# Performance work log

Hardware: AMD Instinct MI355X
Metric: run time of the kernel (lower is better)

## Reference

```python
import jax, jax.numpy as jnp
import numpy as np

N_NODES = 50000
N_EDGES = 800000
N_GRAPHS = 256
C_FEAT = 108
MLP_DIM = 88
OUT_DIM = 100


def setup_inputs() -> dict:
    key = jax.random.key(0)
    ks = jax.random.split(key, 12)
    x = jax.random.normal(ks[0], (N_NODES, C_FEAT), dtype=jnp.float32)
    edge_index = jax.random.randint(ks[1], (2, N_EDGES), 0, N_NODES, dtype=jnp.int64)
    batch = jnp.sort(jax.random.randint(ks[2], (N_NODES,), 0, N_GRAPHS, dtype=jnp.int64))

    def glorot(k, shape):
        fan_in, fan_out = shape
        s = jnp.sqrt(2.0 / (fan_in + fan_out))
        return jax.random.normal(k, shape, dtype=jnp.float32) * s

    return {
        "x": x,
        "edge_index": edge_index,
        "batch": batch,
        # SAGEConv layer 1: lin_l (neighbors, has bias), lin_r (root, no bias)
        "W1l": glorot(ks[3], (C_FEAT, MLP_DIM)),
        "W1r": glorot(ks[4], (C_FEAT, MLP_DIM)),
        "b1": jnp.zeros((MLP_DIM,), jnp.float32),
        "W2l": glorot(ks[5], (MLP_DIM, MLP_DIM)),
        "W2r": glorot(ks[6], (MLP_DIM, MLP_DIM)),
        "b2": jnp.zeros((MLP_DIM,), jnp.float32),
        "W3l": glorot(ks[7], (MLP_DIM, MLP_DIM)),
        "W3r": glorot(ks[8], (MLP_DIM, MLP_DIM)),
        "b3": jnp.zeros((MLP_DIM,), jnp.float32),
        "Wlin": glorot(ks[9], (MLP_DIM, OUT_DIM)),
        "blin": jnp.zeros((OUT_DIM,), jnp.float32),
    }


def _sage_conv(x, src, dst, Wl, Wr, b):
    """PyG SAGEConv(aggr='mean'): out = lin_l(mean_j x_j) + lin_r(x)."""
    n = x.shape[0]
    msg = x[src]  # [E, d] gather from source nodes
    agg = jax.ops.segment_sum(msg, dst, num_segments=n)  # [N, d]
    cnt = jax.ops.segment_sum(jnp.ones((src.shape[0],), x.dtype), dst, num_segments=n)
    agg = agg / jnp.maximum(cnt, 1.0)[:, None]  # scatter-mean
    return agg @ Wl + b + x @ Wr


def reference(x, edge_index, batch, W1l, W1r, b1, W2l, W2r, b2, W3l, W3r, b3, Wlin, blin):
    src, dst = edge_index[0], edge_index[1]
    h = jax.nn.relu(_sage_conv(x, src, dst, W1l, W1r, b1))
    h = jax.nn.relu(_sage_conv(h, src, dst, W2l, W2r, b2))
    h = jax.nn.relu(_sage_conv(h, src, dst, W3l, W3r, b3))
    pooled = jax.ops.segment_sum(h, batch, num_segments=N_GRAPHS)  # global_add_pool
    return pooled @ Wlin + blin  # [n_graphs, 100]
```

## Files before the change

### kernel.cpp

```cpp
#include <hip/hip_runtime.h>
#include <hip/hip_fp16.h>

#define NN 50000
#define NG 256
#define CF 108
#define MD 88
#define OD 100
#define F2 44
#define HP 96
#define HP2 48
#define YLS 96
#define K1P 128
#define NSB 196
#define SBCAP 5120
#define TILE 2048
#define NCH 12

typedef _Float16 f16x8 __attribute__((ext_vector_type(8)));
typedef float f32x4 __attribute__((ext_vector_type(4)));


__global__ __launch_bounds__(256) void prep_kernel(const int* __restrict__ edge, int E,
                                                   int* __restrict__ sbcur,
                                                   unsigned* __restrict__ sbrec,
                                                   const float* __restrict__ x,
                                                   _Float16* __restrict__ xh, int N,
                                                   const float* __restrict__ W1l, const float* __restrict__ W1r,
                                                   const float* __restrict__ W2l, const float* __restrict__ W2r,
                                                   const float* __restrict__ W3l, const float* __restrict__ W3r,
                                                   _Float16* __restrict__ Wct1, _Float16* __restrict__ Wct23,
                                                   int nbin, int nconvx) {
    const int tid = threadIdx.x;
    const int bb  = blockIdx.x;

    if (bb < nbin) {
        __shared__ int bcnt[NSB], boff[NSB], bfill[NSB], gbase[NSB];
        __shared__ int sc[256];
        __shared__ unsigned stag[TILE];
        __shared__ unsigned char stagbin[TILE];
        const int t0  = bb * TILE;
        const int tcnt = min(TILE, E - t0);

        for (int i = tid; i < NSB; i += 256) bcnt[i] = 0;
        __syncthreads();

        unsigned recs[TILE / 256];
        int      bins[TILE / 256];
        #pragma unroll
        for (int j = 0; j < TILE / 256; ++j) {
            const int e = t0 + j * 256 + tid;
            bins[j] = -1;
            if (e < E) {
                const int dst = edge[E + e], src = edge[e];
                bins[j] = dst >> 8;
                recs[j] = ((unsigned)src << 8) | (unsigned)(dst & 255);
                atomicAdd(&bcnt[bins[j]], 1);
            }
        }
        __syncthreads();

        sc[tid] = (tid < NSB) ? bcnt[tid] : 0;
        __syncthreads();
        for (int d = 1; d < 256; d <<= 1) {
            int v = (tid >= d) ? sc[tid - d] : 0;
            __syncthreads();
            sc[tid] += v;
            __syncthreads();
        }
        if (tid < NSB) {
            boff[tid]  = sc[tid] - bcnt[tid];
            bfill[tid] = sc[tid] - bcnt[tid];
            if (bcnt[tid] > 0) gbase[tid] = atomicAdd(&sbcur[tid], bcnt[tid]);
        }
        __syncthreads();

        #pragma unroll
        for (int j = 0; j < TILE / 256; ++j) {
            if (bins[j] >= 0) {
                int pos = atomicAdd(&bfill[bins[j]], 1);
                stag[pos]    = recs[j];
                stagbin[pos] = (unsigned char)bins[j];
            }
        }
        __syncthreads();

        for (int i = tid; i < tcnt; i += 256) {
            const int b   = stagbin[i];
            const int rel = i - boff[b];
            const int gp  = gbase[b] + rel;
            if (gp < SBCAP) sbrec[(size_t)b * SBCAP + gp] = stag[i];
        }
    } else if (bb < nbin + nconvx) {
        const int i = (bb - nbin) * 256 + tid;
        if (i < N * K1P) {
            int n = i >> 7, k = i & (K1P - 1);
            xh[i] = (k < CF) ? (_Float16)x[n * CF + k] : (_Float16)0.f;
        }
    } else {
        const int n1 = 176 * K1P;
        const int n2 = 176 * HP;
        const int idx = (bb - nbin - nconvx) * 256 + tid;
        if (idx < n1) {
            int c = idx / K1P, k = idx - c * K1P;
            float v = (k < CF) ? ((c < MD) ? W1l[k * MD + c] : W1r[k * MD + (c - MD)]) : 0.f;
            Wct1[idx] = (_Float16)v;
        } else if (idx < n1 + 2 * n2) {
            int j = idx - n1;
            const float* Wl = (j < n2) ? W2l : W3l;
            const float* Wr = (j < n2) ? W2r : W3r;
            int jj = (j < n2) ? j : j - n2;
            int c = jj / HP, k = jj - c * HP;
            float v = (k < MD) ? ((c < MD) ? Wl[k * MD + c] : Wr[k * MD + (c - MD)]) : 0.f;
            Wct23[j] = (_Float16)v;
        }
    }
}


__global__ __launch_bounds__(256) void csr256_kernel(const unsigned* __restrict__ sbrec,
                                                     const int* __restrict__ sbcur,
                                                     int* __restrict__ csr,
                                                     int2* __restrict__ off2,
                                                     int* __restrict__ order, int N) {
    __shared__ int hist[256], base[256], offc[256], sc[256];
    __shared__ int dcnt[64], dpos[64];
    const int b = blockIdx.x, tid = threadIdx.x;
    const int cnt = min(sbcur[b], SBCAP);
    const unsigned* rec = sbrec + (size_t)b * SBCAP;

    hist[tid] = 0;
    if (tid < 64) dcnt[tid] = 0;
    __syncthreads();
    for (int r = tid; r < cnt; r += 256) atomicAdd(&hist[rec[r] & 255u], 1);
    __syncthreads();

    sc[tid] = hist[tid];
    __syncthreads();
    for (int d = 1; d < 256; d <<= 1) {
        int v = (tid >= d) ? sc[tid - d] : 0;
        __syncthreads();
        sc[tid] += v;
        __syncthreads();
    }
    base[tid] = sc[tid] - hist[tid];
    offc[tid] = base[tid];
    __syncthreads();

    for (int r = tid; r < cnt; r += 256) {
        const unsigned u = rec[r];
        const int dl = (int)(u & 255u);
        const int pos = atomicAdd(&offc[dl], 1);
        csr[(size_t)b * SBCAP + pos] = (int)(u >> 8);
    }

    const int n = b * 256 + tid;
    const int deg = (n < N) ? min(hist[tid], 63) : 63;
    atomicAdd(&dcnt[deg], 1);
    __syncthreads();
    if (tid < 64) {
        int v = dcnt[tid];
        int incl = v;
        #pragma unroll
        for (int s = 1; s < 64; s <<= 1) {
            int t = __shfl_up(incl, s, 64);
            if (tid >= s) incl += t;
        }
        dpos[tid] = incl - v;
    }
    __syncthreads();
    const int rank = atomicAdd(&dpos[deg], 1);
    order[b * 256 + rank] = (n < N) ? n : -1;

    if (n < N) off2[n] = make_int2(b * SBCAP + base[tid], hist[tid]);
}


template <int KPAD>
__global__ __launch_bounds__(256) void gemm_mfma_kernel(const _Float16* __restrict__ Ah,
                                                        const _Float16* __restrict__ Wct,
                                                        const float* __restrict__ bias,
                                                        _Float16* __restrict__ yl,
                                                        _Float16* __restrict__ yr, int N) {
    const int wave = threadIdx.x >> 6;
    const int lane = threadIdx.x & 63;
    const int r16  = lane & 15;
    const int kg   = lane >> 4;
    const int rbase = blockIdx.x * 128 + wave * 16;

    const int arow0 = min(rbase + r16, N - 1);
    const int arow1 = min(rbase + 64 + r16, N - 1);
    const _Float16* ap0 = Ah + (size_t)arow0 * KPAD + kg * 8;
    const _Float16* ap1 = Ah + (size_t)arow1 * KPAD + kg * 8;

    f32x4 acc[2][11];
    #pragma unroll
    for (int q = 0; q < 2; ++q)
        #pragma unroll
        for (int t = 0; t < 11; ++t) acc[q][t] = (f32x4){0.f, 0.f, 0.f, 0.f};

    #pragma unroll
    for (int ks = 0; ks < KPAD / 32; ++ks) {
        f16x8 af0 = *(const f16x8*)(ap0 + ks * 32);
        f16x8 af1 = *(const f16x8*)(ap1 + ks * 32);
        #pragma unroll
        for (int t = 0; t < 11; ++t) {
            const _Float16* bp = Wct + (size_t)(t * 16 + r16) * KPAD + ks * 32 + kg * 8;
            f16x8 bf = *(const f16x8*)bp;
            acc[0][t] = __builtin_amdgcn_mfma_f32_16x16x32_f16(af0, bf, acc[0][t], 0, 0, 0);
            acc[1][t] = __builtin_amdgcn_mfma_f32_16x16x32_f16(af1, bf, acc[1][t], 0, 0, 0);
        }
    }

    #pragma unroll
    for (int q = 0; q < 2; ++q) {
        const int orow0 = rbase + q * 64 + kg * 4;
        #pragma unroll
        for (int t = 0; t < 11; ++t) {
            const int c = t * 16 + r16;
            const bool isr = (c >= MD);
            const float bv = isr ? bias[c - MD] : 0.f;
            _Float16* dst = isr ? (yr + (c - MD)) : (yl + c);
            const int st = isr ? MD : YLS;
            #pragma unroll
            for (int r = 0; r < 4; ++r) {
                const int row = orow0 + r;
                if (row < N) dst[(size_t)row * st] = (_Float16)(acc[q][t][r] + bv);
            }
        }
    }
}


__global__ void agg_kernel(const _Float16* __restrict__ yl, const _Float16* __restrict__ yr,
                           const int2* __restrict__ off2, const int* __restrict__ csr,
                           const int* __restrict__ order,
                           _Float16* __restrict__ h, int total) {
    int idx = blockIdx.x * blockDim.x + threadIdx.x;
    if (idx >= total) return;
    int slot = idx / NCH;
    int c = idx - slot * NCH;
    const int n = order[slot];
    if (n < 0) return;
    if (c >= 11) {
        *(f16x8*)(h + (size_t)n * HP + 88) = (f16x8)(_Float16)0.f;
        return;
    }
    const int2 o = off2[n];
    const int s = o.x, e = o.x + o.y;
    float a0[8] = {0,0,0,0,0,0,0,0}, a1[8] = {0,0,0,0,0,0,0,0};
    float a2[8] = {0,0,0,0,0,0,0,0}, a3[8] = {0,0,0,0,0,0,0,0};
    const size_t cof = (size_t)c * 8;
    int i = s;
    for (; i + 7 < e; i += 8) {
        f16x8 v0 = *(const f16x8*)(yl + (size_t)csr[i]     * YLS + cof);
        f16x8 v1 = *(const f16x8*)(yl + (size_t)csr[i + 1] * YLS + cof);
        f16x8 v2 = *(const f16x8*)(yl + (size_t)csr[i + 2] * YLS + cof);
        f16x8 v3 = *(const f16x8*)(yl + (size_t)csr[i + 3] * YLS + cof);
        f16x8 v4 = *(const f16x8*)(yl + (size_t)csr[i + 4] * YLS + cof);
        f16x8 v5 = *(const f16x8*)(yl + (size_t)csr[i + 5] * YLS + cof);
        f16x8 v6 = *(const f16x8*)(yl + (size_t)csr[i + 6] * YLS + cof);
        f16x8 v7 = *(const f16x8*)(yl + (size_t)csr[i + 7] * YLS + cof);
        #pragma unroll
        for (int j = 0; j < 8; ++j) {
            a0[j] += (float)v0[j] + (float)v1[j];
            a1[j] += (float)v2[j] + (float)v3[j];
            a2[j] += (float)v4[j] + (float)v5[j];
            a3[j] += (float)v6[j] + (float)v7[j];
        }
    }
    for (; i + 1 < e; i += 2) {
        f16x8 v0 = *(const f16x8*)(yl + (size_t)csr[i]     * YLS + cof);
        f16x8 v1 = *(const f16x8*)(yl + (size_t)csr[i + 1] * YLS + cof);
        #pragma unroll
        for (int j = 0; j < 8; ++j) {
            a0[j] += (float)v0[j];
            a1[j] += (float)v1[j];
        }
    }
    if (i < e) {
        f16x8 v0 = *(const f16x8*)(yl + (size_t)csr[i] * YLS + cof);
        #pragma unroll
        for (int j = 0; j < 8; ++j) a0[j] += (float)v0[j];
    }
    const float inv = 1.0f / (float)max(o.y, 1);
    const f16x8 r = *(const f16x8*)(yr + (size_t)n * MD + cof);
    f16x8 outv;
    #pragma unroll
    for (int j = 0; j < 8; ++j) {
        float v = (a0[j] + a1[j] + a2[j] + a3[j]) * inv + (float)r[j];
        outv[j] = (_Float16)fmaxf(v, 0.f);
    }
    *(f16x8*)(h + (size_t)n * HP + cof) = outv;
}


__global__ __launch_bounds__(256) void pool_final_kernel(const __half2* __restrict__ h2,
                                                         const int* __restrict__ batch,
                                                         const float* __restrict__ Wlin,
                                                         const float* __restrict__ blin,
                                                         float* __restrict__ out, int N) {
    __shared__ float red[4][F2][2];
    __shared__ float pooled[MD];
    __shared__ int range[2];
    const int g    = blockIdx.x;
    const int tid  = threadIdx.x;
    const int w    = tid >> 6;
    const int lane = tid & 63;

    if (tid < 2) {
        const int tgt = g + tid;
        int lo = 0, hi = N;
        while (lo < hi) {
            int mid = (lo + hi) >> 1;
            if (batch[mid] < tgt) lo = mid + 1; else hi = mid;
        }
        range[tid] = lo;
    }
    __syncthreads();
    const int s = range[0], e = range[1];

    float ax0 = 0.f, ay0 = 0.f, ax1 = 0.f, ay1 = 0.f;
    if (lane < F2) {
        int n = s + w;
        for (; n + 4 < e; n += 8) {
            __half2 v0 = h2[(size_t)n * HP2 + lane];
            __half2 v1 = h2[(size_t)(n + 4) * HP2 + lane];
            ax0 += __low2float(v0); ay0 += __high2float(v0);
            ax1 += __low2float(v1); ay1 += __high2float(v1);
        }
        if (n < e) {
            __half2 v0 = h2[(size_t)n * HP2 + lane];
            ax0 += __low2float(v0); ay0 += __high2float(v0);
        }
        red[w][lane][0] = ax0 + ax1;
        red[w][lane][1] = ay0 + ay1;
    }
    __syncthreads();
    if (tid < F2) {
        pooled[2 * tid]     = red[0][tid][0] + red[1][tid][0] + red[2][tid][0] + red[3][tid][0];
        pooled[2 * tid + 1] = red[0][tid][1] + red[1][tid][1] + red[2][tid][1] + red[3][tid][1];
    }
    __syncthreads();
    if (tid < OD) {
        float acc = blin[tid];
        #pragma unroll 8
        for (int f = 0; f < MD; ++f)
            acc = fmaf(pooled[f], Wlin[f * OD + tid], acc);
        out[(size_t)g * OD + tid] = acc;
    }
}


extern "C" void kernel_launch(void* const* d_in, const int* in_sizes, int n_in,
                              void* d_out, int out_size, void* d_ws, size_t ws_size,
                              hipStream_t stream) {
    const float* x     = (const float*)d_in[0];
    const int*   edge  = (const int*)d_in[1];
    const int*   batch = (const int*)d_in[2];
    const float* W1l = (const float*)d_in[3];
    const float* W1r = (const float*)d_in[4];
    const float* b1  = (const float*)d_in[5];
    const float* W2l = (const float*)d_in[6];
    const float* W2r = (const float*)d_in[7];
    const float* b2  = (const float*)d_in[8];
    const float* W3l = (const float*)d_in[9];
    const float* W3r = (const float*)d_in[10];
    const float* b3  = (const float*)d_in[11];
    const float* Wlin = (const float*)d_in[12];
    const float* blin = (const float*)d_in[13];
    float* out = (float*)d_out;

    const int N = in_sizes[0] / CF;
    const int E = in_sizes[1] / 2;

    char* ws = (char*)d_ws;
    auto alloc = [&](size_t bytes) -> void* {
        void* p = (void*)ws;
        ws += (bytes + 255) & ~(size_t)255;
        return p;
    };
    int*       sbcur   = (int*)alloc((size_t)NSB * 4);
    unsigned*  sbrec   = (unsigned*)alloc((size_t)NSB * SBCAP * 4);
    int*       csr     = (int*)alloc((size_t)NSB * SBCAP * 4);
    int2*      off2    = (int2*)alloc((size_t)N * 8);
    int*       order   = (int*)alloc((size_t)NSB * 256 * 4);
    _Float16*  Wct1    = (_Float16*)alloc((size_t)176 * K1P * 2);
    _Float16*  Wct23   = (_Float16*)alloc((size_t)2 * 176 * HP * 2);
    _Float16*  xh      = (_Float16*)alloc((size_t)N * K1P * 2);
    _Float16*  yl      = (_Float16*)alloc((size_t)N * YLS * 2);
    _Float16*  yr      = (_Float16*)alloc((size_t)N * MD * 2);
    _Float16*  h       = (_Float16*)alloc((size_t)N * HP * 2);

    const int nbin   = (E + TILE - 1) / TILE;
    const int nconvx = (N * K1P + 255) / 256;
    const int nwct   = (176 * K1P + 2 * 176 * HP + 255) / 256;

    hipMemsetAsync(sbcur, 0, (size_t)NSB * 4, stream);
    prep_kernel<<<nbin + nconvx + nwct, 256, 0, stream>>>(
        edge, E, sbcur, sbrec, x, xh, N,
        W1l, W1r, W2l, W2r, W3l, W3r, Wct1, Wct23, nbin, nconvx);
    csr256_kernel<<<NSB, 256, 0, stream>>>(sbrec, sbcur, csr, off2, order, N);

    const int gemm_blocks = (N + 127) / 128;
    const int agg_total   = NSB * 256 * NCH;
    const int agg_blocks  = (agg_total + 255) / 256;

    gemm_mfma_kernel<K1P><<<gemm_blocks, 256, 0, stream>>>(xh, Wct1, b1, yl, yr, N);
    agg_kernel<<<agg_blocks, 256, 0, stream>>>(yl, yr, off2, csr, order, h, agg_total);

    gemm_mfma_kernel<HP><<<gemm_blocks, 256, 0, stream>>>(h, Wct23, b2, yl, yr, N);
    agg_kernel<<<agg_blocks, 256, 0, stream>>>(yl, yr, off2, csr, order, h, agg_total);

    gemm_mfma_kernel<HP><<<gemm_blocks, 256, 0, stream>>>(h, Wct23 + (size_t)176 * HP, b3, yl, yr, N);
    agg_kernel<<<agg_blocks, 256, 0, stream>>>(yl, yr, off2, csr, order, h, agg_total);

    pool_final_kernel<<<NG, 256, 0, stream>>>((const __half2*)h, batch, Wlin, blin, out, N);
}
```

Baseline: 203.0 us.

## Fuse mean aggregation into following layer GEMM via shared-memory tile

Adds an agg_gemm_kernel that aggregates neighbor features for a 128-node block into LDS and then runs the next layer's MFMA GEMM on that tile, replacing the separate agg and gemm launches for layers 2 and 3. Ping-pong yl/yr buffers avoid read/write hazards across layers. This removes the h round-trip through global memory and two launches, but drops the degree-sorted order used for load balancing, so blocks with high-degree nodes may straggle.

```diff
diff --git a/kernel.cpp b/kernel.cpp
--- a/kernel.cpp
+++ b/kernel.cpp
@@ -9,6 +9,7 @@
 #define F2 44
 #define HP 96
 #define HP2 48
+#define HLS 104
 #define YLS 96
 #define K1P 128
 #define NSB 196
@@ -175,6 +176,131 @@
 }
 
 
+__device__ __forceinline__ f16x8 agg_chunk(const _Float16* __restrict__ yl,
+                                           const _Float16* __restrict__ yr,
+                                           int2 o, int n, size_t cof,
+                                           const int* __restrict__ csr) {
+    const int s = o.x, e = o.x + o.y;
+    float a0[8] = {0,0,0,0,0,0,0,0}, a1[8] = {0,0,0,0,0,0,0,0};
+    float a2[8] = {0,0,0,0,0,0,0,0}, a3[8] = {0,0,0,0,0,0,0,0};
+    int i = s;
+    for (; i + 7 < e; i += 8) {
+        f16x8 v0 = *(const f16x8*)(yl + (size_t)csr[i]     * YLS + cof);
+        f16x8 v1 = *(const f16x8*)(yl + (size_t)csr[i + 1] * YLS + cof);
+        f16x8 v2 = *(const f16x8*)(yl + (size_t)csr[i + 2] * YLS + cof);
+        f16x8 v3 = *(const f16x8*)(yl + (size_t)csr[i + 3] * YLS + cof);
+        f16x8 v4 = *(const f16x8*)(yl + (size_t)csr[i + 4] * YLS + cof);
+        f16x8 v5 = *(const f16x8*)(yl + (size_t)csr[i + 5] * YLS + cof);
+        f16x8 v6 = *(const f16x8*)(yl + (size_t)csr[i + 6] * YLS + cof);
+        f16x8 v7 = *(const f16x8*)(yl + (size_t)csr[i + 7] * YLS + cof);
+        #pragma unroll
+        for (int j = 0; j < 8; ++j) {
+            a0[j] += (float)v0[j] + (float)v1[j];
+            a1[j] += (float)v2[j] + (float)v3[j];
+            a2[j] += (float)v4[j] + (float)v5[j];
+            a3[j] += (float)v6[j] + (float)v7[j];
+        }
+    }
+    for (; i + 1 < e; i += 2) {
+        f16x8 v0 = *(const f16x8*)(yl + (size_t)csr[i]     * YLS + cof);
+        f16x8 v1 = *(const f16x8*)(yl + (size_t)csr[i + 1] * YLS + cof);
+        #pragma unroll
+        for (int j = 0; j < 8; ++j) { a0[j] += (float)v0[j]; a1[j] += (float)v1[j]; }
+    }
+    if (i < e) {
+        f16x8 v0 = *(const f16x8*)(yl + (size_t)csr[i] * YLS + cof);
+        #pragma unroll
+        for (int j = 0; j < 8; ++j) a0[j] += (float)v0[j];
+    }
+    const float inv = 1.0f / (float)max(o.y, 1);
+    const f16x8 r = *(const f16x8*)(yr + (size_t)n * MD + cof);
+    f16x8 outv;
+    #pragma unroll
+    for (int j = 0; j < 8; ++j) {
+        float v = (a0[j] + a1[j] + a2[j] + a3[j]) * inv + (float)r[j];
+        outv[j] = (_Float16)fmaxf(v, 0.f);
+    }
+    return outv;
+}
+
+
+__global__ __launch_bounds__(256) void agg_gemm_kernel(const _Float16* __restrict__ yl_in,
+                                                       const _Float16* __restrict__ yr_in,
+                                                       const int2* __restrict__ off2,
+                                                       const int* __restrict__ csr,
+                                                       const _Float16* __restrict__ Wct,
+                                                       const float* __restrict__ bias,
+                                                       _Float16* __restrict__ yl_out,
+                                                       _Float16* __restrict__ yr_out, int N) {
+    __shared__ _Float16 hl[128 * HLS];
+    const int tid = threadIdx.x;
+    const int nb0 = blockIdx.x * 128;
+
+    #pragma unroll
+    for (int k = 0; k < 6; ++k) {
+        const int item = k * 256 + tid;
+        const int node = item / NCH;
+        const int c = item - node * NCH;
+        const int n = nb0 + node;
+        if (c >= 11 || n >= N) {
+            const int off = (c >= 11) ? 88 : c * 8;
+            *(f16x8*)(hl + (size_t)node * HLS + off) = (f16x8)(_Float16)0.f;
+            continue;
+        }
+        const size_t cof = (size_t)c * 8;
+        f16x8 outv = agg_chunk(yl_in, yr_in, off2[n], n, cof, csr);
+        *(f16x8*)(hl + (size_t)node * HLS + cof) = outv;
+    }
+    __syncthreads();
+
+    const int wave = tid >> 6;
+    const int lane = tid & 63;
+    const int r16  = lane & 15;
+    const int kg   = lane >> 4;
+    const int rbase = nb0 + wave * 16;
+
+    const _Float16* ap0 = hl + (size_t)(wave * 16 + r16) * HLS + kg * 8;
+    const _Float16* ap1 = hl + (size_t)(wave * 16 + 64 + r16) * HLS + kg * 8;
+
+    f32x4 acc[2][11];
+    #pragma unroll
+    for (int q = 0; q < 2; ++q)
+        #pragma unroll
+        for (int t = 0; t < 11; ++t) acc[q][t] = (f32x4){0.f, 0.f, 0.f, 0.f};
+
+    #pragma unroll
+    for (int ks = 0; ks < HP / 32; ++ks) {
+        f16x8 af0 = *(const f16x8*)(ap0 + ks * 32);
+        f16x8 af1 = *(const f16x8*)(ap1 + ks * 32);
+        #pragma unroll
+        for (int t = 0; t < 11; ++t) {
+            const _Float16* bp = Wct + (size_t)(t * 16 + r16) * HP + ks * 32 + kg * 8;
+            f16x8 bf = *(const f16x8*)bp;
+            acc[0][t] = __builtin_amdgcn_mfma_f32_16x16x32_f16(af0, bf, acc[0][t], 0, 0, 0);
+            acc[1][t] = __builtin_amdgcn_mfma_f32_16x16x32_f16(af1, bf, acc[1][t], 0, 0, 0);
+        }
+    }
+
+    #pragma unroll
+    for (int q = 0; q < 2; ++q) {
+        const int orow0 = rbase + q * 64 + kg * 4;
+        #pragma unroll
+        for (int t = 0; t < 11; ++t) {
+            const int c = t * 16 + r16;
+            const bool isr = (c >= MD);
+            const float bv = isr ? bias[c - MD] : 0.f;
+            _Float16* dst = isr ? (yr_out + (c - MD)) : (yl_out + c);
+            const int st = isr ? MD : YLS;
+            #pragma unroll
+            for (int r = 0; r < 4; ++r) {
+                const int row = orow0 + r;
+                if (row < N) dst[(size_t)row * st] = (_Float16)(acc[q][t][r] + bv);
+            }
+        }
+    }
+}
+
+
 template <int KPAD>
 __global__ __launch_bounds__(256) void gemm_mfma_kernel(const _Float16* __restrict__ Ah,
                                                         const _Float16* __restrict__ Wct,
@@ -245,51 +371,8 @@
         *(f16x8*)(h + (size_t)n * HP + 88) = (f16x8)(_Float16)0.f;
         return;
     }
-    const int2 o = off2[n];
-    const int s = o.x, e = o.x + o.y;
-    float a0[8] = {0,0,0,0,0,0,0,0}, a1[8] = {0,0,0,0,0,0,0,0};
-    float a2[8] = {0,0,0,0,0,0,0,0}, a3[8] = {0,0,0,0,0,0,0,0};
     const size_t cof = (size_t)c * 8;
-    int i = s;
-    for (; i + 7 < e; i += 8) {
-        f16x8 v0 = *(const f16x8*)(yl + (size_t)csr[i]     * YLS + cof);
-        f16x8 v1 = *(const f16x8*)(yl + (size_t)csr[i + 1] * YLS + cof);
-        f16x8 v2 = *(const f16x8*)(yl + (size_t)csr[i + 2] * YLS + cof);
-        f16x8 v3 = *(const f16x8*)(yl + (size_t)csr[i + 3] * YLS + cof);
-        f16x8 v4 = *(const f16x8*)(yl + (size_t)csr[i + 4] * YLS + cof);
-        f16x8 v5 = *(const f16x8*)(yl + (size_t)csr[i + 5] * YLS + cof);
-        f16x8 v6 = *(const f16x8*)(yl + (size_t)csr[i + 6] * YLS + cof);
-        f16x8 v7 = *(const f16x8*)(yl + (size_t)csr[i + 7] * YLS + cof);
-        #pragma unroll
-        for (int j = 0; j < 8; ++j) {
-            a0[j] += (float)v0[j] + (float)v1[j];
-            a1[j] += (float)v2[j] + (float)v3[j];
-            a2[j] += (float)v4[j] + (float)v5[j];
-            a3[j] += (float)v6[j] + (float)v7[j];
-        }
-    }
-    for (; i + 1 < e; i += 2) {
-        f16x8 v0 = *(const f16x8*)(yl + (size_t)csr[i]     * YLS + cof);
-        f16x8 v1 = *(const f16x8*)(yl + (size_t)csr[i + 1] * YLS + cof);
-        #pragma unroll
-        for (int j = 0; j < 8; ++j) {
-            a0[j] += (float)v0[j];
-            a1[j] += (float)v1[j];
-        }
-    }
-    if (i < e) {
-        f16x8 v0 = *(const f16x8*)(yl + (size_t)csr[i] * YLS + cof);
-        #pragma unroll
-        for (int j = 0; j < 8; ++j) a0[j] += (float)v0[j];
-    }
-    const float inv = 1.0f / (float)max(o.y, 1);
-    const f16x8 r = *(const f16x8*)(yr + (size_t)n * MD + cof);
-    f16x8 outv;
-    #pragma unroll
-    for (int j = 0; j < 8; ++j) {
-        float v = (a0[j] + a1[j] + a2[j] + a3[j]) * inv + (float)r[j];
-        outv[j] = (_Float16)fmaxf(v, 0.f);
-    }
+    f16x8 outv = agg_chunk(yl, yr, off2[n], n, cof, csr);
     *(f16x8*)(h + (size_t)n * HP + cof) = outv;
 }
 
@@ -387,8 +470,10 @@
     _Float16*  Wct1    = (_Float16*)alloc((size_t)176 * K1P * 2);
     _Float16*  Wct23   = (_Float16*)alloc((size_t)2 * 176 * HP * 2);
     _Float16*  xh      = (_Float16*)alloc((size_t)N * K1P * 2);
-    _Float16*  yl      = (_Float16*)alloc((size_t)N * YLS * 2);
-    _Float16*  yr      = (_Float16*)alloc((size_t)N * MD * 2);
+    _Float16*  ylA     = (_Float16*)alloc((size_t)N * YLS * 2);
+    _Float16*  yrA     = (_Float16*)alloc((size_t)N * MD * 2);
+    _Float16*  ylB     = (_Float16*)alloc((size_t)N * YLS * 2);
+    _Float16*  yrB     = (_Float16*)alloc((size_t)N * MD * 2);
     _Float16*  h       = (_Float16*)alloc((size_t)N * HP * 2);
 
     const int nbin   = (E + TILE - 1) / TILE;
@@ -401,18 +486,14 @@
         W1l, W1r, W2l, W2r, W3l, W3r, Wct1, Wct23, nbin, nconvx);
     csr256_kernel<<<NSB, 256, 0, stream>>>(sbrec, sbcur, csr, off2, order, N);
 
-    const int gemm_blocks = (N + 127) / 128;
-    const int agg_total   = NSB * 256 * NCH;
-    const int agg_blocks  = (agg_total + 255) / 256;
-
-    gemm_mfma_kernel<K1P><<<gemm_blocks, 256, 0, stream>>>(xh, Wct1, b1, yl, yr, N);
-    agg_kernel<<<agg_blocks, 256, 0, stream>>>(yl, yr, off2, csr, order, h, agg_total);
-
-    gemm_mfma_kernel<HP><<<gemm_blocks, 256, 0, stream>>>(h, Wct23, b2, yl, yr, N);
-    agg_kernel<<<agg_blocks, 256, 0, stream>>>(yl, yr, off2, csr, order, h, agg_total);
-
-    gemm_mfma_kernel<HP><<<gemm_blocks, 256, 0, stream>>>(h, Wct23 + (size_t)176 * HP, b3, yl, yr, N);
-    agg_kernel<<<agg_blocks, 256, 0, stream>>>(yl, yr, off2, csr, order, h, agg_total);
-
+    const int row_blocks = (N + 127) / 128;
+    const int agg_total  = NSB * 256 * NCH;
+    const int agg_blocks = (agg_total + 255) / 256;
+
+    gemm_mfma_kernel<K1P><<<row_blocks, 256, 0, stream>>>(xh, Wct1, b1, ylA, yrA, N);
+    agg_gemm_kernel<<<row_blocks, 256, 0, stream>>>(ylA, yrA, off2, csr, Wct23, b2, ylB, yrB, N);
+    agg_gemm_kernel<<<row_blocks, 256, 0, stream>>>(ylB, yrB, off2, csr,
+                                                    Wct23 + (size_t)176 * HP, b3, ylA, yrA, N);
+    agg_kernel<<<agg_blocks, 256, 0, stream>>>(ylA, yrA, off2, csr, order, h, agg_total);
     pool_final_kernel<<<NG, 256, 0, stream>>>((const __half2*)h, batch, Wlin, blin, out, N);
 }
```

After: 204.6 us. Within noise of the previous version (+0.8%).

## Stage GEMM outputs through LDS for vectorized stores and halve rows per block

Applied to the files above, without the earlier changes.

The GEMM kernel now computes 64 rows per block instead of 128, one 16-row MFMA tile per wave, which doubles the number of blocks. Results are written to a shared-memory tile first and then stored to yl/yr as contiguous 16-byte vectors, replacing scattered 2-byte stores. This is meant to improve write coalescing and occupancy, at the cost of fewer reuses of each loaded weight fragment per block and an extra LDS round trip. The aggregation body is also moved into a helper function with no change in behaviour.

```diff
diff --git a/kernel.cpp b/kernel.cpp
--- a/kernel.cpp
+++ b/kernel.cpp
@@ -11,6 +11,7 @@
 #define HP2 48
 #define YLS 96
 #define K1P 128
+#define CLS 184
 #define NSB 196
 #define SBCAP 5120
 #define TILE 2048
@@ -181,53 +182,99 @@
                                                         const float* __restrict__ bias,
                                                         _Float16* __restrict__ yl,
                                                         _Float16* __restrict__ yr, int N) {
+    __shared__ _Float16 cst[64 * CLS];
     const int wave = threadIdx.x >> 6;
     const int lane = threadIdx.x & 63;
     const int r16  = lane & 15;
     const int kg   = lane >> 4;
-    const int rbase = blockIdx.x * 128 + wave * 16;
-
-    const int arow0 = min(rbase + r16, N - 1);
-    const int arow1 = min(rbase + 64 + r16, N - 1);
-    const _Float16* ap0 = Ah + (size_t)arow0 * KPAD + kg * 8;
-    const _Float16* ap1 = Ah + (size_t)arow1 * KPAD + kg * 8;
-
-    f32x4 acc[2][11];
+    const int rbase = blockIdx.x * 64 + wave * 16;
+
+    const int arow = min(rbase + r16, N - 1);
+    const _Float16* ap = Ah + (size_t)arow * KPAD + kg * 8;
+
+    f32x4 acc[11];
     #pragma unroll
-    for (int q = 0; q < 2; ++q)
-        #pragma unroll
-        for (int t = 0; t < 11; ++t) acc[q][t] = (f32x4){0.f, 0.f, 0.f, 0.f};
+    for (int t = 0; t < 11; ++t) acc[t] = (f32x4){0.f, 0.f, 0.f, 0.f};
 
     #pragma unroll
     for (int ks = 0; ks < KPAD / 32; ++ks) {
-        f16x8 af0 = *(const f16x8*)(ap0 + ks * 32);
-        f16x8 af1 = *(const f16x8*)(ap1 + ks * 32);
+        f16x8 af = *(const f16x8*)(ap + ks * 32);
         #pragma unroll
         for (int t = 0; t < 11; ++t) {
             const _Float16* bp = Wct + (size_t)(t * 16 + r16) * KPAD + ks * 32 + kg * 8;
             f16x8 bf = *(const f16x8*)bp;
-            acc[0][t] = __builtin_amdgcn_mfma_f32_16x16x32_f16(af0, bf, acc[0][t], 0, 0, 0);
-            acc[1][t] = __builtin_amdgcn_mfma_f32_16x16x32_f16(af1, bf, acc[1][t], 0, 0, 0);
-        }
-    }
-
+            acc[t] = __builtin_amdgcn_mfma_f32_16x16x32_f16(af, bf, acc[t], 0, 0, 0);
+        }
+    }
+
+    const int lrow0 = wave * 16 + kg * 4;
     #pragma unroll
-    for (int q = 0; q < 2; ++q) {
-        const int orow0 = rbase + q * 64 + kg * 4;
-        #pragma unroll
-        for (int t = 0; t < 11; ++t) {
-            const int c = t * 16 + r16;
-            const bool isr = (c >= MD);
-            const float bv = isr ? bias[c - MD] : 0.f;
-            _Float16* dst = isr ? (yr + (c - MD)) : (yl + c);
-            const int st = isr ? MD : YLS;
-            #pragma unroll
-            for (int r = 0; r < 4; ++r) {
-                const int row = orow0 + r;
-                if (row < N) dst[(size_t)row * st] = (_Float16)(acc[q][t][r] + bv);
-            }
-        }
-    }
+    for (int t = 0; t < 11; ++t) {
+        const int c = t * 16 + r16;
+        const float bv = (c >= MD) ? bias[c - MD] : 0.f;
+        #pragma unroll
+        for (int r = 0; r < 4; ++r)
+            cst[(lrow0 + r) * CLS + c] = (_Float16)(acc[t][r] + bv);
+    }
+    __syncthreads();
+
+    for (int it = lane; it < 16 * 22; it += 64) {
+        const int rr = it / 22;
+        const int cc = it - rr * 22;
+        const int row = rbase + rr;
+        if (row >= N) continue;
+        f16x8 v = *(const f16x8*)(cst + (wave * 16 + rr) * CLS + cc * 8);
+        if (cc < 11) *(f16x8*)(yl + (size_t)row * YLS + cc * 8) = v;
+        else         *(f16x8*)(yr + (size_t)row * MD + (cc - 11) * 8) = v;
+    }
+}
+
+
+__device__ __forceinline__ f16x8 agg_chunk(const _Float16* __restrict__ yl,
+                                           const _Float16* __restrict__ yr,
+                                           int2 o, int n, size_t cof,
+                                           const int* __restrict__ csr) {
+    const int s = o.x, e = o.x + o.y;
+    float a0[8] = {0,0,0,0,0,0,0,0}, a1[8] = {0,0,0,0,0,0,0,0};
+    float a2[8] = {0,0,0,0,0,0,0,0}, a3[8] = {0,0,0,0,0,0,0,0};
+    int i = s;
+    for (; i + 7 < e; i += 8) {
+        f16x8 v0 = *(const f16x8*)(yl + (size_t)csr[i]     * YLS + cof);
+        f16x8 v1 = *(const f16x8*)(yl + (size_t)csr[i + 1] * YLS + cof);
+        f16x8 v2 = *(const f16x8*)(yl + (size_t)csr[i + 2] * YLS + cof);
+        f16x8 v3 = *(const f16x8*)(yl + (size_t)csr[i + 3] * YLS + cof);
+        f16x8 v4 = *(const f16x8*)(yl + (size_t)csr[i + 4] * YLS + cof);
+        f16x8 v5 = *(const f16x8*)(yl + (size_t)csr[i + 5] * YLS + cof);
+        f16x8 v6 = *(const f16x8*)(yl + (size_t)csr[i + 6] * YLS + cof);
+        f16x8 v7 = *(const f16x8*)(yl + (size_t)csr[i + 7] * YLS + cof);
+        #pragma unroll
+        for (int j = 0; j < 8; ++j) {
+            a0[j] += (float)v0[j] + (float)v1[j];
+            a1[j] += (float)v2[j] + (float)v3[j];
+            a2[j] += (float)v4[j] + (float)v5[j];
+            a3[j] += (float)v6[j] + (float)v7[j];
+        }
+    }
+    for (; i + 1 < e; i += 2) {
+        f16x8 v0 = *(const f16x8*)(yl + (size_t)csr[i]     * YLS + cof);
+        f16x8 v1 = *(const f16x8*)(yl + (size_t)csr[i + 1] * YLS + cof);
+        #pragma unroll
+        for (int j = 0; j < 8; ++j) { a0[j] += (float)v0[j]; a1[j] += (float)v1[j]; }
+    }
+    if (i < e) {
+        f16x8 v0 = *(const f16x8*)(yl + (size_t)csr[i] * YLS + cof);
+        #pragma unroll
+        for (int j = 0; j < 8; ++j) a0[j] += (float)v0[j];
+    }
+    const float inv = 1.0f / (float)max(o.y, 1);
+    const f16x8 r = *(const f16x8*)(yr + (size_t)n * MD + cof);
+    f16x8 outv;
+    #pragma unroll
+    for (int j = 0; j < 8; ++j) {
+        float v = (a0[j] + a1[j] + a2[j] + a3[j]) * inv + (float)r[j];
+        outv[j] = (_Float16)fmaxf(v, 0.f);
+    }
+    return outv;
 }
 
 
@@ -245,51 +292,8 @@
         *(f16x8*)(h + (size_t)n * HP + 88) = (f16x8)(_Float16)0.f;
         return;
     }
-    const int2 o = off2[n];
-    const int s = o.x, e = o.x + o.y;
-    float a0[8] = {0,0,0,0,0,0,0,0}, a1[8] = {0,0,0,0,0,0,0,0};
-    float a2[8] = {0,0,0,0,0,0,0,0}, a3[8] = {0,0,0,0,0,0,0,0};
     const size_t cof = (size_t)c * 8;
-    int i = s;
-    for (; i + 7 < e; i += 8) {
-        f16x8 v0 = *(const f16x8*)(yl + (size_t)csr[i]     * YLS + cof);
-        f16x8 v1 = *(const f16x8*)(yl + (size_t)csr[i + 1] * YLS + cof);
-        f16x8 v2 = *(const f16x8*)(yl + (size_t)csr[i + 2] * YLS + cof);
-        f16x8 v3 = *(const f16x8*)(yl + (size_t)csr[i + 3] * YLS + cof);
-        f16x8 v4 = *(const f16x8*)(yl + (size_t)csr[i + 4] * YLS + cof);
-        f16x8 v5 = *(const f16x8*)(yl + (size_t)csr[i + 5] * YLS + cof);
-        f16x8 v6 = *(const f16x8*)(yl + (size_t)csr[i + 6] * YLS + cof);
-        f16x8 v7 = *(const f16x8*)(yl + (size_t)csr[i + 7] * YLS + cof);
-        #pragma unroll
-        for (int j = 0; j < 8; ++j) {
-            a0[j] += (float)v0[j] + (float)v1[j];
-            a1[j] += (float)v2[j] + (float)v3[j];
-            a2[j] += (float)v4[j] + (float)v5[j];
-            a3[j] += (float)v6[j] + (float)v7[j];
-        }
-    }
-    for (; i + 1 < e; i += 2) {
-        f16x8 v0 = *(const f16x8*)(yl + (size_t)csr[i]     * YLS + cof);
-        f16x8 v1 = *(const f16x8*)(yl + (size_t)csr[i + 1] * YLS + cof);
-        #pragma unroll
-        for (int j = 0; j < 8; ++j) {
-            a0[j] += (float)v0[j];
-            a1[j] += (float)v1[j];
-        }
-    }
-    if (i < e) {
-        f16x8 v0 = *(const f16x8*)(yl + (size_t)csr[i] * YLS + cof);
-        #pragma unroll
-        for (int j = 0; j < 8; ++j) a0[j] += (float)v0[j];
-    }
-    const float inv = 1.0f / (float)max(o.y, 1);
-    const f16x8 r = *(const f16x8*)(yr + (size_t)n * MD + cof);
-    f16x8 outv;
-    #pragma unroll
-    for (int j = 0; j < 8; ++j) {
-        float v = (a0[j] + a1[j] + a2[j] + a3[j]) * inv + (float)r[j];
-        outv[j] = (_Float16)fmaxf(v, 0.f);
-    }
+    f16x8 outv = agg_chunk(yl, yr, off2[n], n, cof, csr);
     *(f16x8*)(h + (size_t)n * HP + cof) = outv;
 }
 
@@ -401,7 +405,7 @@
         W1l, W1r, W2l, W2r, W3l, W3r, Wct1, Wct23, nbin, nconvx);
     csr256_kernel<<<NSB, 256, 0, stream>>>(sbrec, sbcur, csr, off2, order, N);
 
-    const int gemm_blocks = (N + 127) / 128;
+    const int gemm_blocks = (N + 63) / 64;
     const int agg_total   = NSB * 256 * NCH;
     const int agg_blocks  = (agg_total + 255) / 256;
 
```

New measurement: 205.6 us. No clear change (+1.3%).
